# Optimization experiments

Measured on AMD Instinct MI355X. Metric: run time of the kernel, lower is better.

Reference implementation:

```python
import jax, jax.numpy as jnp
import numpy as np

N_NODES = 100000
N_EDGES = 1600000
IN_CH = 50


def setup_inputs() -> dict:
    key = jax.random.key(0)
    ks = jax.random.split(key, 6)
    x = jax.random.normal(ks[0], (N_NODES, IN_CH), dtype=jnp.float32)
    edge_index = jax.random.randint(ks[1], (2, N_EDGES), 0, N_NODES, dtype=jnp.int32)
    # Glorot-ish scaled weights
    W1 = jax.random.normal(ks[2], (2 * IN_CH, 64), dtype=jnp.float32) * (1.0 / np.sqrt(2 * IN_CH))
    b1 = jnp.zeros((64,), jnp.float32)
    W2 = jax.random.normal(ks[3], (2 * 64, 32), dtype=jnp.float32) * (1.0 / np.sqrt(2 * 64))
    b2 = jnp.zeros((32,), jnp.float32)
    W3 = jax.random.normal(ks[4], (32, 1), dtype=jnp.float32) * (1.0 / np.sqrt(32))
    b3 = jnp.zeros((1,), jnp.float32)
    return {"x": x, "edge_index": edge_index, "W1": W1, "b1": b1,
            "W2": W2, "b2": b2, "W3": W3, "b3": b3}


def _sage_conv(x, src, dst, W, b, n_nodes):
    # mean aggregation of neighbor (source) features onto target nodes
    msg = x[src]                                             # [E, d] gather
    agg = jax.ops.segment_sum(msg, dst, num_segments=n_nodes)  # [N, d]
    cnt = jax.ops.segment_sum(jnp.ones(src.shape[0], x.dtype), dst,
                              num_segments=n_nodes)            # [N]
    mean = agg / jnp.maximum(cnt, 1.0)[:, None]
    h = jnp.concatenate([x, mean], axis=-1)                  # concat=True
    return h @ W + b


def reference(x, edge_index, W1, b1, W2, b2, W3, b3):
    src, dst = edge_index[0], edge_index[1]
    n = x.shape[0]
    h = jax.nn.relu(_sage_conv(x, src, dst, W1, b1, n))
    h = jax.nn.relu(_sage_conv(h, src, dst, W2, b2, n))
    return h @ W3 + b3  # [N, 1]
```

## Files before the change

### kernel.cpp

```cpp
#include <hip/hip_runtime.h>
#include <hip/hip_bf16.h>

#define N_NODES 100000
#define N_EDGES 1600000
#define IN_CH 50
#define NPB 256
#define NB ((N_NODES + NPB - 1) / NPB)
#define CAPLOG 13
#define EPB 4096
#define NBLK_A ((N_EDGES + EPB - 1) / EPB)
#define PAD_BLOCKS ((N_NODES * 64) / 1024)

__global__ __launch_bounds__(1024) void bin_pad_kernel(
    const int* __restrict__ src, const int* __restrict__ dst,
    int* __restrict__ cursor_rel, unsigned* __restrict__ binned,
    const float* __restrict__ x, unsigned short* __restrict__ xb) {
    if (blockIdx.x >= NBLK_A) {
        int t = (blockIdx.x - NBLK_A) * 1024 + threadIdx.x;
        int n = t >> 6, c = t & 63;
        float v = (c < IN_CH) ? x[n * IN_CH + c] : 0.0f;
        __hip_bfloat16 hb = __float2bfloat16(v);
        xb[t] = *(unsigned short*)&hb;
        return;
    }
    __shared__ unsigned payl[EPB];
    __shared__ unsigned short bktl[EPB];
    __shared__ int bc[NB];
    __shared__ int boff[NB];
    int t = threadIdx.x;
    if (t < NB) bc[t] = 0;
    __syncthreads();
    int e0 = blockIdx.x * EPB;
    int ne = min(e0 + EPB, N_EDGES) - e0;
    for (int i = t; i < ne; i += 1024) {
        int d = dst[e0 + i];
        int s = src[e0 + i];
        payl[i] = ((unsigned)(d & 255) << 17) | (unsigned)s;
        bktl[i] = (unsigned short)(d >> 8);
        atomicAdd(&bc[d >> 8], 1);
    }
    __syncthreads();
    if (t < NB) {
        int v = bc[t];
        int rel = v ? atomicAdd(&cursor_rel[t], v) : 0;
        boff[t] = (t << CAPLOG) + rel;
        bc[t] = 0;
    }
    __syncthreads();
    for (int i = t; i < ne; i += 1024) {
        int b = bktl[i];
        int k = atomicAdd(&bc[b], 1);
        binned[boff[b] + k] = payl[i];
    }
}

__global__ __launch_bounds__(1024) void bucket_fine(
    const unsigned* __restrict__ binned, const int* __restrict__ cursor_rel,
    int* __restrict__ cnt, int* __restrict__ row_start, int* __restrict__ csr_src) {
    __shared__ unsigned srt[1 << CAPLOG];
    __shared__ int lcnt[NPB];
    __shared__ int lofs[NPB];
    __shared__ int sc[NPB];
    int t = threadIdx.x;
    int b = blockIdx.x;
    int nbase = b * NPB;
    int bbase = b << CAPLOG;
    int ecnt  = cursor_rel[b];
    if (t < NPB) lcnt[t] = 0;
    __syncthreads();
    for (int i = t; i < ecnt; i += 1024)
        atomicAdd(&lcnt[(binned[bbase + i] >> 17) & 255], 1);
    __syncthreads();
    int v = (t < NPB) ? lcnt[t] : 0;
    if (t < NPB) sc[t] = v;
    __syncthreads();
    for (int off = 1; off < NPB; off <<= 1) {
        int tmp = (t < NPB && t >= off) ? sc[t - off] : 0;
        __syncthreads();
        if (t < NPB) sc[t] += tmp;
        __syncthreads();
    }
    if (t < NPB) {
        int excl = sc[t] - v;
        lofs[t] = excl;
        int n = nbase + t;
        if (n < N_NODES) { cnt[n] = v; row_start[n] = bbase + excl; }
    }
    __syncthreads();
    for (int i = t; i < ecnt; i += 1024) {
        unsigned p = binned[bbase + i];
        int d = (int)((p >> 17) & 255);
        int k = atomicAdd(&lofs[d], 1);
        srt[k] = p & 0x1FFFFu;
    }
    __syncthreads();
    for (int i = t; i < ecnt; i += 1024)
        csr_src[bbase + i] = (int)srt[i];
}

__device__ __forceinline__ void upadd8(float* a, uint4 v, float p) {
    a[0] = fmaf(p, __uint_as_float(v.x << 16), a[0]);
    a[1] = fmaf(p, __uint_as_float(v.x & 0xffff0000u), a[1]);
    a[2] = fmaf(p, __uint_as_float(v.y << 16), a[2]);
    a[3] = fmaf(p, __uint_as_float(v.y & 0xffff0000u), a[3]);
    a[4] = fmaf(p, __uint_as_float(v.z << 16), a[4]);
    a[5] = fmaf(p, __uint_as_float(v.z & 0xffff0000u), a[5]);
    a[6] = fmaf(p, __uint_as_float(v.w << 16), a[6]);
    a[7] = fmaf(p, __uint_as_float(v.w & 0xffff0000u), a[7]);
}

#define WAVE_LDS_FENCE() __asm__ volatile("s_waitcnt lgkmcnt(0)" ::: "memory")

__device__ __forceinline__ void gather2(
    const unsigned short* __restrict__ featb, const int* __restrict__ csr_src,
    const int* __restrict__ row_start, const int* __restrict__ cnt,
    int nb, int lane, float acc[2][8]) {
    int g  = lane >> 3;
    int cw = (lane & 7) * 8;
    int start[2], deg[2], sv[2];
    #pragma unroll
    for (int i = 0; i < 2; ++i) {
        start[i] = row_start[nb + i];
        deg[i]   = cnt[nb + i];
        #pragma unroll
        for (int c = 0; c < 8; ++c) acc[i][c] = 0.f;
    }
    int dmax = max(deg[0], deg[1]);
    #pragma unroll
    for (int i = 0; i < 2; ++i)
        sv[i] = (lane < deg[i]) ? csr_src[start[i] + lane] : 0;

    #pragma unroll
    for (int cb = 0; cb < 64; cb += 16) {
        if (cb >= dmax) break;
        int s00 = __shfl(sv[0], cb + g);
        int s01 = __shfl(sv[0], cb + 8 + g);
        int s10 = __shfl(sv[1], cb + g);
        int s11 = __shfl(sv[1], cb + 8 + g);
        uint4 v00 = *(const uint4*)(featb + s00 * 64 + cw);
        uint4 v01 = *(const uint4*)(featb + s01 * 64 + cw);
        uint4 v10 = *(const uint4*)(featb + s10 * 64 + cw);
        uint4 v11 = *(const uint4*)(featb + s11 * 64 + cw);
        int rem0 = deg[0] - cb;
        int rem1 = deg[1] - cb;
        upadd8(acc[0], v00, (g < rem0) ? 1.f : 0.f);
        upadd8(acc[0], v01, (g + 8 < rem0) ? 1.f : 0.f);
        upadd8(acc[1], v10, (g < rem1) ? 1.f : 0.f);
        upadd8(acc[1], v11, (g + 8 < rem1) ? 1.f : 0.f);
    }
    if (dmax > 64) {
        for (int i = 0; i < 2; ++i) {
            for (int c0 = 64; c0 < deg[i]; c0 += 64) {
                int rem = deg[i] - c0; if (rem > 64) rem = 64;
                int sx = (lane < rem) ? csr_src[start[i] + c0 + lane] : 0;
                for (int cb = 0; cb < rem; cb += 16) {
                    int s0 = __shfl(sx, cb + g);
                    int s1 = __shfl(sx, cb + 8 + g);
                    float p0 = (cb + g < rem) ? 1.f : 0.f;
                    float p1 = (cb + 8 + g < rem) ? 1.f : 0.f;
                    uint4 v0 = *(const uint4*)(featb + s0 * 64 + cw);
                    uint4 v1 = *(const uint4*)(featb + s1 * 64 + cw);
                    upadd8(acc[i], v0, p0);
                    upadd8(acc[i], v1, p1);
                }
            }
        }
    }
    #pragma unroll
    for (int i = 0; i < 2; ++i) {
        float inv = 1.0f / fmaxf((float)deg[i], 1.0f);
        #pragma unroll
        for (int c = 0; c < 8; ++c) {
            float t = acc[i][c];
            t += __shfl_xor(t, 8);
            t += __shfl_xor(t, 16);
            t += __shfl_xor(t, 32);
            acc[i][c] = t * inv;
        }
    }
}

__device__ __forceinline__ float bf16u(unsigned short u) {
    return __uint_as_float(((unsigned)u) << 16);
}

__global__ __launch_bounds__(256, 8) void layer1_fused(
    const unsigned short* __restrict__ xb,
    const int* __restrict__ csr_src, const int* __restrict__ row_start,
    const int* __restrict__ cnt, const float* __restrict__ W1,
    const float* __restrict__ b1, unsigned short* __restrict__ h1b) {
    int wv   = threadIdx.x >> 6;
    int lane = threadIdx.x & 63;
    int nb   = (blockIdx.x * 4 + wv) * 2;

    float acc[2][8];
    gather2(xb, csr_src, row_start, cnt, nb, lane, acc);

    __shared__ __align__(16) float selfF[4][2][64];
    __shared__ __align__(16) float meanF[4][2][64];
    #pragma unroll
    for (int i = 0; i < 2; ++i) {
        selfF[wv][i][lane] = bf16u(xb[((nb + i) << 6) + lane]);
        if (lane < 8) {
            *(float4*)&meanF[wv][i][lane * 8] =
                make_float4(acc[i][0], acc[i][1], acc[i][2], acc[i][3]);
            *(float4*)&meanF[wv][i][lane * 8 + 4] =
                make_float4(acc[i][4], acc[i][5], acc[i][6], acc[i][7]);
        }
    }
    WAVE_LDS_FENCE();

    float ao[2];
    float bb = b1[lane];
    #pragma unroll
    for (int i = 0; i < 2; ++i) ao[i] = bb;
    #pragma unroll
    for (int k = 0; k < IN_CH; ++k) {
        float w = W1[k * 64 + lane];
        #pragma unroll
        for (int i = 0; i < 2; ++i) ao[i] = fmaf(selfF[wv][i][k], w, ao[i]);
    }
    #pragma unroll
    for (int k = 0; k < IN_CH; ++k) {
        float w = W1[(IN_CH + k) * 64 + lane];
        #pragma unroll
        for (int i = 0; i < 2; ++i) ao[i] = fmaf(meanF[wv][i][k], w, ao[i]);
    }
    #pragma unroll
    for (int i = 0; i < 2; ++i) {
        float r = fmaxf(ao[i], 0.f);
        __hip_bfloat16 hb = __float2bfloat16(r);
        h1b[((nb + i) << 6) + lane] = *(unsigned short*)&hb;
    }
}

__global__ __launch_bounds__(256) void transform_w2(
    const unsigned short* __restrict__ h1b,
    const float* __restrict__ W2, const float* __restrict__ b2,
    unsigned short* __restrict__ y2b, float* __restrict__ yselff) {
    __shared__ __align__(16) float hrowF[4][4][64];
    int t    = threadIdx.x;
    int wv   = t >> 6;
    int lane = t & 63;
    int nb4  = blockIdx.x * 16 + wv * 4;

    {
        int in = lane >> 4, q = lane & 15;
        uint2 hv = *(const uint2*)(h1b + (nb4 + in) * 64 + q * 4);
        float4 f;
        f.x = __uint_as_float(hv.x << 16);
        f.y = __uint_as_float(hv.x & 0xffff0000u);
        f.z = __uint_as_float(hv.y << 16);
        f.w = __uint_as_float(hv.y & 0xffff0000u);
        *(float4*)&hrowF[wv][in][q * 4] = f;
    }
    WAVE_LDS_FENCE();

    int jj  = lane & 31;
    int sel = lane >> 5;
    const float* Wp = W2 + sel * 64 * 32 + jj;
    float a[4] = {0.f, 0.f, 0.f, 0.f};
    #pragma unroll
    for (int k = 0; k < 64; ++k) {
        float w = Wp[k * 32];
        #pragma unroll
        for (int i = 0; i < 4; ++i)
            a[i] = fmaf(hrowF[wv][i][k], w, a[i]);
    }
    if (sel == 0) {
        float bb = b2[jj];
        #pragma unroll
        for (int i = 0; i < 4; ++i)
            yselff[(nb4 + i) * 32 + jj] = a[i] + bb;
    } else {
        #pragma unroll
        for (int i = 0; i < 4; ++i) {
            __hip_bfloat16 hb = __float2bfloat16(a[i]);
            y2b[(nb4 + i) * 32 + jj] = *(unsigned short*)&hb;
        }
    }
}

__global__ __launch_bounds__(256, 8) void layer23_fused(
    const unsigned short* __restrict__ y2b,
    const int* __restrict__ csr_src, const int* __restrict__ row_start,
    const int* __restrict__ cnt, const float* __restrict__ yselff,
    const float* __restrict__ W3, const float* __restrict__ b3,
    float* __restrict__ out) {
    int wv   = threadIdx.x >> 6;
    int lane = threadIdx.x & 63;
    int nb   = (blockIdx.x * 4 + wv) * 2;
    int g  = lane >> 2;
    int cw = (lane & 3) * 8;

    int start[2], deg[2], sv[2];
    float acc[2][8];
    #pragma unroll
    for (int i = 0; i < 2; ++i) {
        start[i] = row_start[nb + i];
        deg[i]   = cnt[nb + i];
        #pragma unroll
        for (int c = 0; c < 8; ++c) acc[i][c] = 0.f;
    }
    int dmax = max(deg[0], deg[1]);
    #pragma unroll
    for (int i = 0; i < 2; ++i)
        sv[i] = (lane < deg[i]) ? csr_src[start[i] + lane] : 0;

    #pragma unroll
    for (int cb = 0; cb < 64; cb += 32) {
        if (cb >= dmax) break;
        int s00 = __shfl(sv[0], cb + g);
        int s01 = __shfl(sv[0], cb + 16 + g);
        int s10 = __shfl(sv[1], cb + g);
        int s11 = __shfl(sv[1], cb + 16 + g);
        uint4 v00 = *(const uint4*)(y2b + s00 * 32 + cw);
        uint4 v01 = *(const uint4*)(y2b + s01 * 32 + cw);
        uint4 v10 = *(const uint4*)(y2b + s10 * 32 + cw);
        uint4 v11 = *(const uint4*)(y2b + s11 * 32 + cw);
        int rem0 = deg[0] - cb;
        int rem1 = deg[1] - cb;
        upadd8(acc[0], v00, (g < rem0) ? 1.f : 0.f);
        upadd8(acc[0], v01, (g + 16 < rem0) ? 1.f : 0.f);
        upadd8(acc[1], v10, (g < rem1) ? 1.f : 0.f);
        upadd8(acc[1], v11, (g + 16 < rem1) ? 1.f : 0.f);
    }
    if (dmax > 64) {
        for (int i = 0; i < 2; ++i) {
            for (int c0 = 64; c0 < deg[i]; c0 += 64) {
                int rem = deg[i] - c0; if (rem > 64) rem = 64;
                int sx = (lane < rem) ? csr_src[start[i] + c0 + lane] : 0;
                for (int cb = 0; cb < rem; cb += 32) {
                    int s0 = __shfl(sx, cb + g);
                    int s1 = __shfl(sx, cb + 16 + g);
                    float p0 = (cb + g < rem) ? 1.f : 0.f;
                    float p1 = (cb + 16 + g < rem) ? 1.f : 0.f;
                    uint4 v0 = *(const uint4*)(y2b + s0 * 32 + cw);
                    uint4 v1 = *(const uint4*)(y2b + s1 * 32 + cw);
                    upadd8(acc[i], v0, p0);
                    upadd8(acc[i], v1, p1);
                }
            }
        }
    }

    __shared__ __align__(16) float aggF[4][2][32];
    #pragma unroll
    for (int i = 0; i < 2; ++i) {
        float inv = 1.0f / fmaxf((float)deg[i], 1.0f);
        #pragma unroll
        for (int c = 0; c < 8; ++c) {
            float t = acc[i][c];
            t += __shfl_xor(t, 4);
            t += __shfl_xor(t, 8);
            t += __shfl_xor(t, 16);
            t += __shfl_xor(t, 32);
            acc[i][c] = t * inv;
        }
    }
    if (lane < 4) {
        #pragma unroll
        for (int i = 0; i < 2; ++i) {
            *(float4*)&aggF[wv][i][lane * 8] =
                make_float4(acc[i][0], acc[i][1], acc[i][2], acc[i][3]);
            *(float4*)&aggF[wv][i][lane * 8 + 4] =
                make_float4(acc[i][4], acc[i][5], acc[i][6], acc[i][7]);
        }
    }
    WAVE_LDS_FENCE();

    int hh = lane >> 5;
    int j  = lane & 31;
    float pre = yselff[(nb + hh) * 32 + j] + aggF[wv][hh][j];
    float v0 = fmaxf(pre, 0.f) * W3[j];
    #pragma unroll
    for (int off = 1; off <= 16; off <<= 1)
        v0 += __shfl_xor(v0, off);
    if (j == 0)
        out[nb + hh] = v0 + b3[0];
}

extern "C" void kernel_launch(void* const* d_in, const int* in_sizes, int n_in,
                              void* d_out, int out_size, void* d_ws, size_t ws_size,
                              hipStream_t stream) {
    const float* x   = (const float*)d_in[0];
    const int*   ei  = (const int*)d_in[1];
    const int*   src = ei;
    const int*   dst = ei + N_EDGES;
    const float* W1  = (const float*)d_in[2];
    const float* b1  = (const float*)d_in[3];
    const float* W2  = (const float*)d_in[4];
    const float* b2  = (const float*)d_in[5];
    const float* W3  = (const float*)d_in[6];
    const float* b3  = (const float*)d_in[7];
    float* out = (float*)d_out;

    char* ws = (char*)d_ws;
    auto align = [](size_t v) { return (v + 255) & ~(size_t)255; };
    size_t o = 0;
    int* cursor_rel = (int*)(ws + o); o = align(o + 512 * 4);
    int* cnt       = (int*)(ws + o); o = align(o + (size_t)N_NODES * 4);
    int* row_start = (int*)(ws + o); o = align(o + (size_t)N_NODES * 4);
    unsigned* binned = (unsigned*)(ws + o); o = align(o + ((size_t)NB << CAPLOG) * 4);
    int* csr_src   = (int*)(ws + o); o = align(o + ((size_t)NB << CAPLOG) * 4);
    unsigned short* xb  = (unsigned short*)(ws + o); o = align(o + (size_t)N_NODES * 64 * 2);
    unsigned short* h1b = (unsigned short*)(ws + o); o = align(o + (size_t)N_NODES * 64 * 2);
    unsigned short* y2b = (unsigned short*)(ws + o); o = align(o + (size_t)N_NODES * 32 * 2);
    float* yselff = (float*)(ws + o); o = align(o + (size_t)N_NODES * 32 * 4);

    (void)hipMemsetAsync(cursor_rel, 0, 512 * sizeof(int), stream);

    bin_pad_kernel<<<NBLK_A + PAD_BLOCKS, 1024, 0, stream>>>(src, dst, cursor_rel,
                                                             binned, x, xb);
    bucket_fine<<<NB, 1024, 0, stream>>>(binned, cursor_rel, cnt, row_start, csr_src);

    layer1_fused<<<N_NODES / 8, 256, 0, stream>>>(xb, csr_src, row_start, cnt,
                                                  W1, b1, h1b);
    transform_w2<<<N_NODES / 16, 256, 0, stream>>>(h1b, W2, b2, y2b, yselff);
    layer23_fused<<<N_NODES / 8, 256, 0, stream>>>(y2b, csr_src, row_start, cnt,
                                                   yselff, W3, b3, out);
}
```

Measured before the change: 232.8 us.

## Keep edge payloads in registers, reuse atomic ranks, vectorize bf16 padding

Both binning kernels now keep their edge payloads and the rank returned by the first shared-memory atomic in registers, 8 per thread. The scatter pass reuses that rank instead of issuing a second atomic and re-reading the payload from LDS or global memory. EPB doubles to 8192 so each block handles 8 edges per thread, which halves the global cursor atomics. The pad path converts two floats per thread and writes packed 32-bit words. The risk is that bucket_fine assumes at most 8192 edges per bucket, which fits CAPLOG but silently drops any overflow; the removed LDS arrays are traded for extra register pressure.

Measured after the change: 224.3 us, median of 2. 3.7% less time.

```diff
diff --git a/kernel.cpp b/kernel.cpp
--- a/kernel.cpp
+++ b/kernel.cpp
@@ -7,9 +7,9 @@
 #define NPB 256
 #define NB ((N_NODES + NPB - 1) / NPB)
 #define CAPLOG 13
-#define EPB 4096
+#define EPB 8192
 #define NBLK_A ((N_EDGES + EPB - 1) / EPB)
-#define PAD_BLOCKS ((N_NODES * 64) / 1024)
+#define PAD_BLOCKS ((N_NODES * 32) / 1024)
 
 __global__ __launch_bounds__(1024) void bin_pad_kernel(
     const int* __restrict__ src, const int* __restrict__ dst,
@@ -17,14 +17,17 @@
     const float* __restrict__ x, unsigned short* __restrict__ xb) {
     if (blockIdx.x >= NBLK_A) {
         int t = (blockIdx.x - NBLK_A) * 1024 + threadIdx.x;
-        int n = t >> 6, c = t & 63;
-        float v = (c < IN_CH) ? x[n * IN_CH + c] : 0.0f;
-        __hip_bfloat16 hb = __float2bfloat16(v);
-        xb[t] = *(unsigned short*)&hb;
+        int n = t >> 5, q = t & 31;
+        unsigned u = 0;
+        if (q < 25) {
+            float2 v = *(const float2*)(x + n * IN_CH + q * 2);
+            __hip_bfloat16 lo = __float2bfloat16(v.x);
+            __hip_bfloat16 hi = __float2bfloat16(v.y);
+            u = ((unsigned)*(unsigned short*)&hi << 16) | *(unsigned short*)&lo;
+        }
+        ((unsigned*)xb)[t] = u;
         return;
     }
-    __shared__ unsigned payl[EPB];
-    __shared__ unsigned short bktl[EPB];
     __shared__ int bc[NB];
     __shared__ int boff[NB];
     int t = threadIdx.x;
@@ -32,25 +35,30 @@
     __syncthreads();
     int e0 = blockIdx.x * EPB;
     int ne = min(e0 + EPB, N_EDGES) - e0;
-    for (int i = t; i < ne; i += 1024) {
-        int d = dst[e0 + i];
-        int s = src[e0 + i];
-        payl[i] = ((unsigned)(d & 255) << 17) | (unsigned)s;
-        bktl[i] = (unsigned short)(d >> 8);
-        atomicAdd(&bc[d >> 8], 1);
+    unsigned payl[8];
+    int bkt[8], rnk[8];
+    #pragma unroll
+    for (int r = 0; r < 8; ++r) {
+        int i = t + r * 1024;
+        if (i < ne) {
+            int d = dst[e0 + i];
+            payl[r] = ((unsigned)(d & 255) << 17) | (unsigned)src[e0 + i];
+            bkt[r]  = d >> 8;
+            rnk[r]  = atomicAdd(&bc[bkt[r]], 1);
+        }
     }
     __syncthreads();
     if (t < NB) {
         int v = bc[t];
         int rel = v ? atomicAdd(&cursor_rel[t], v) : 0;
         boff[t] = (t << CAPLOG) + rel;
-        bc[t] = 0;
-    }
-    __syncthreads();
-    for (int i = t; i < ne; i += 1024) {
-        int b = bktl[i];
-        int k = atomicAdd(&bc[b], 1);
-        binned[boff[b] + k] = payl[i];
+    }
+    __syncthreads();
+    #pragma unroll
+    for (int r = 0; r < 8; ++r) {
+        int i = t + r * 1024;
+        if (i < ne)
+            binned[boff[bkt[r]] + rnk[r]] = payl[r];
     }
 }
 
@@ -68,8 +76,16 @@
     int ecnt  = cursor_rel[b];
     if (t < NPB) lcnt[t] = 0;
     __syncthreads();
-    for (int i = t; i < ecnt; i += 1024)
-        atomicAdd(&lcnt[(binned[bbase + i] >> 17) & 255], 1);
+    unsigned pay[8];
+    int rnk[8];
+    #pragma unroll
+    for (int r = 0; r < 8; ++r) {
+        int i = t + r * 1024;
+        if (i < ecnt) {
+            pay[r] = binned[bbase + i];
+            rnk[r] = atomicAdd(&lcnt[(pay[r] >> 17) & 255], 1);
+        }
+    }
     __syncthreads();
     int v = (t < NPB) ? lcnt[t] : 0;
     if (t < NPB) sc[t] = v;
@@ -87,11 +103,11 @@
         if (n < N_NODES) { cnt[n] = v; row_start[n] = bbase + excl; }
     }
     __syncthreads();
-    for (int i = t; i < ecnt; i += 1024) {
-        unsigned p = binned[bbase + i];
-        int d = (int)((p >> 17) & 255);
-        int k = atomicAdd(&lofs[d], 1);
-        srt[k] = p & 0x1FFFFu;
+    #pragma unroll
+    for (int r = 0; r < 8; ++r) {
+        int i = t + r * 1024;
+        if (i < ecnt)
+            srt[lofs[(pay[r] >> 17) & 255] + rnk[r]] = pay[r] & 0x1FFFFu;
     }
     __syncthreads();
     for (int i = t; i < ecnt; i += 1024)
```
